# Performance work log

Hardware: AMD Instinct MI355X
Metric: run time of the kernel (lower is better)

The kernel has to match this reference:

```python
import jax, jax.numpy as jnp
import numpy as np

B, T, NF, D, H = 4, 32, 256, 512, 8
DK = D // H


def setup_inputs() -> dict:
    key = jax.random.key(0)
    ks = jax.random.split(key, 10)
    x = jax.random.normal(ks[0], (B, T, NF, D), dtype=jnp.float32)
    adj = jax.random.randint(ks[1], (NF, NF), 0, 2, dtype=jnp.int32)
    adj = adj.at[jnp.arange(NF), jnp.arange(NF)].set(1)  # self-loops avoid all-masked rows
    s = 1.0 / np.sqrt(D)
    Wq = jax.random.normal(ks[2], (D, D), dtype=jnp.float32) * s
    Wk = jax.random.normal(ks[3], (D, D), dtype=jnp.float32) * s
    Wv = jax.random.normal(ks[4], (D, D), dtype=jnp.float32) * s
    Wo = jax.random.normal(ks[5], (D, D), dtype=jnp.float32) * s
    bq = jnp.zeros((D,), jnp.float32)
    bk = jnp.zeros((D,), jnp.float32)
    bv = jnp.zeros((D,), jnp.float32)
    bo = jnp.zeros((D,), jnp.float32)
    return {"x": x, "adj": adj, "Wq": Wq, "bq": bq, "Wk": Wk, "bk": bk,
            "Wv": Wv, "bv": bv, "Wo": Wo, "bo": bo}


def reference(x, adj, Wq, bq, Wk, bk, Wv, bv, Wo, bo):
    b, t, nf, d = x.shape
    q = x @ Wq.T + bq
    k = x @ Wk.T + bk
    v = x @ Wv.T + bv
    # split heads: [B,T,Nf,H,dk]
    qh = q.reshape(b, t, nf, H, DK)
    kh = k.reshape(b, t, nf, H, DK)
    vh = v.reshape(b, t, nf, H, DK)
    scores = jnp.einsum('btihd,btjhd->bthij', qh, kh) / jnp.sqrt(jnp.float32(DK))
    mask = (adj > 0)  # [Nf,Nf], broadcast over b,t,h
    scores = jnp.where(mask[None, None, None], scores, jnp.float32(-jnp.inf))
    attn = jax.nn.softmax(scores, axis=-1)  # dropout is identity in eval
    out = jnp.einsum('bthij,btjhd->btihd', attn, vh).reshape(b, t, nf, d)
    return out @ Wo.T + bo
```

## Files before the change

### kernel.cpp

```cpp
#include <hip/hip_runtime.h>

#define NF 256
#define H_ 8
#define M_ 32768

typedef _Float16 f16;
typedef _Float16 f16x8 __attribute__((ext_vector_type(8)));
typedef float f32x4 __attribute__((ext_vector_type(4)));
typedef unsigned short u16x8 __attribute__((ext_vector_type(8)));
typedef unsigned int u32x2 __attribute__((ext_vector_type(2)));
typedef unsigned int u32x4 __attribute__((ext_vector_type(4)));

#define GLOAD16(src, dst) \
  __builtin_amdgcn_global_load_lds((const __attribute__((address_space(1))) void*)(src), \
                                   (__attribute__((address_space(3))) void*)(dst), 16, 0, 0)

#define LDS_FENCE() do { asm volatile("s_waitcnt lgkmcnt(0)" ::: "memory"); \
                         __builtin_amdgcn_sched_barrier(0); } while (0)
#define SBAR() asm volatile("s_barrier" ::: "memory")


__device__ __forceinline__ void stageHT(const f16* __restrict__ g, int r0, int k0,
                                        f16* ldst, int wave, int lane) {
    const int key = lane >> 3;
    const int colsw = k0 + (((lane & 7) ^ key) << 3);
#pragma unroll
    for (int i = 0; i < 2; ++i) {
        int r = i * 64 + wave * 8 + key;
        GLOAD16(g + (size_t)(r0 + r) * 512 + colsw, ldst + (i * 64 + wave * 8) * 64);
    }
}

__device__ __forceinline__ void gemm256_core(const f16* __restrict__ A, const f16* __restrict__ W,
                                             int m0, int n0, f16* lds,
                                             f32x4 (&acc)[8][4], int wave, int lane) {
    const int wr = wave & 1, wc = wave >> 1;
    const int l15 = lane & 15, l4 = lane >> 4;
    stageHT(W, n0,        0, lds + 16384, wave, lane);
    stageHT(W, n0 + 128,  0, lds + 24576, wave, lane);
    stageHT(A, m0,        0, lds,         wave, lane);
    stageHT(A, m0 + 128,  0, lds + 8192,  wave, lane);
    stageHT(W, n0,       64, lds + 32768 + 16384, wave, lane);
    stageHT(W, n0 + 128, 64, lds + 32768 + 24576, wave, lane);
    asm volatile("s_waitcnt vmcnt(4)" ::: "memory");
    SBAR();
#pragma unroll
    for (int t = 0; t < 8; ++t) {
        f16* bufA = lds + (t & 1) * 32768;
        f16* bufB = bufA + 16384;
        f16* nA   = lds + ((t & 1) ^ 1) * 32768;
        f16x8 bfr[4][2];
#pragma unroll
        for (int j = 0; j < 4; ++j)
#pragma unroll
            for (int kk = 0; kk < 2; ++kk) {
                int rb = wc * 64 + j * 16 + l15;
                bfr[j][kk] = *reinterpret_cast<const f16x8*>(
                    bufB + rb * 64 + ((((kk << 2) + l4) ^ (rb & 7)) << 3));
            }
#pragma unroll
        for (int q = 0; q < 4; ++q) {
            f16x8 afr[2][2];
#pragma unroll
            for (int rf = 0; rf < 2; ++rf)
#pragma unroll
                for (int kk = 0; kk < 2; ++kk) {
                    int ra = wr * 128 + q * 32 + rf * 16 + l15;
                    afr[rf][kk] = *reinterpret_cast<const f16x8*>(
                        bufA + ra * 64 + ((((kk << 2) + l4) ^ (ra & 7)) << 3));
                }
            if (q == 0 && t < 7) stageHT(A, m0,       (t + 1) * 64, nA,          wave, lane);
            if (q == 1 && t < 7) stageHT(A, m0 + 128, (t + 1) * 64, nA + 8192,   wave, lane);
            if (q == 2 && t < 6) stageHT(W, n0,       (t + 2) * 64, bufB,        wave, lane);
            if (q == 3 && t < 6) stageHT(W, n0 + 128, (t + 2) * 64, bufB + 8192, wave, lane);
            SBAR();
            LDS_FENCE();
            __builtin_amdgcn_s_setprio(1);
#pragma unroll
            for (int rf = 0; rf < 2; ++rf)
#pragma unroll
                for (int j = 0; j < 4; ++j)
#pragma unroll
                    for (int kk = 0; kk < 2; ++kk)
                        acc[q * 2 + rf][j] = __builtin_amdgcn_mfma_f32_16x16x32_f16(
                            afr[rf][kk], bfr[j][kk], acc[q * 2 + rf][j], 0, 0, 0);
            __builtin_amdgcn_s_setprio(0);
            if (q < 3) SBAR();
        }
        if (t < 6) { asm volatile("s_waitcnt vmcnt(4)" ::: "memory"); }
        else       { asm volatile("s_waitcnt vmcnt(0)" ::: "memory"); }
        SBAR();
    }
}


#define QSCALE 0.1803368801111204f

__global__ void prep_all(const float* __restrict__ x, f16* __restrict__ xh,
                         const float* __restrict__ Wq, const float* __restrict__ Wk,
                         const float* __restrict__ Wv, const float* __restrict__ Wo,
                         const float* __restrict__ bq, const float* __restrict__ bk,
                         const float* __restrict__ bv, const int* __restrict__ adj,
                         f16* __restrict__ Wh, f16* __restrict__ Woh,
                         float* __restrict__ biasAll, unsigned long long* __restrict__ bmask) {
    if (blockIdx.x < 2048) {
        int idx = blockIdx.x * 256 + threadIdx.x;
        for (; idx < M_ * 512 / 8; idx += 2048 * 256) {
            const float4* s = reinterpret_cast<const float4*>(x + (size_t)idx * 8);
            float4 v0 = s[0], v1 = s[1];
            f16x8 o;
            o[0] = (f16)v0.x; o[1] = (f16)v0.y; o[2] = (f16)v0.z; o[3] = (f16)v0.w;
            o[4] = (f16)v1.x; o[5] = (f16)v1.y; o[6] = (f16)v1.z; o[7] = (f16)v1.w;
            *reinterpret_cast<f16x8*>(xh + (size_t)idx * 8) = o;
        }
        return;
    }
    const int tid = (blockIdx.x - 2048) * 256 + threadIdx.x;
    {
        const float* s; f16* d; float sc = 1.0f;
        int pp = tid >> 15, off = tid & 32767;
        if (pp == 0)      { s = Wq; d = Wh;              sc = QSCALE; }
        else if (pp == 1) { s = Wk; d = Wh + 512 * 512; }
        else if (pp == 2) { s = Wv; d = Wh + 2 * 512 * 512; }
        else              { s = Wo; d = Woh; }
        const float4* sv4 = reinterpret_cast<const float4*>(s + (size_t)off * 8);
        float4 v0 = sv4[0], v1 = sv4[1];
        f16x8 o;
        o[0] = (f16)(v0.x * sc); o[1] = (f16)(v0.y * sc);
        o[2] = (f16)(v0.z * sc); o[3] = (f16)(v0.w * sc);
        o[4] = (f16)(v1.x * sc); o[5] = (f16)(v1.y * sc);
        o[6] = (f16)(v1.z * sc); o[7] = (f16)(v1.w * sc);
        *reinterpret_cast<f16x8*>(d + (size_t)off * 8) = o;
    }
    if (tid < 1536) {
        float v = (tid < 512) ? QSCALE * bq[tid] : (tid < 1024) ? bk[tid - 512] : bv[tid - 1024];
        biasAll[tid] = v;
    }
    if (tid < 65536) {
        unsigned long long bal = __ballot(adj[tid] > 0);
        if ((tid & 63) == 0) bmask[tid >> 6] = bal;
    }
}


__global__ __launch_bounds__(512) void qkv_gemm(const f16* __restrict__ A, const f16* __restrict__ W,
                                                const float* __restrict__ biasAll,
                                                f16* __restrict__ out, f16* __restrict__ vT) {
    __shared__ __align__(16) f16 lds[65536];
    const int tt = threadIdx.x, wave = tt >> 6, lane = tt & 63;
    const int lb = blockIdx.x, xcd = lb & 7, idx = lb >> 3;
    const int m0 = (xcd * 16 + idx / 6) * 256;
    const int n0 = (idx % 6) * 256;
    f32x4 acc[8][4] = {};
    gemm256_core(A, W, m0, n0, lds, acc, wave, lane);

    const int wr = wave & 1, wc = wave >> 1;
    const int l15 = lane & 15, l4 = lane >> 4;
    f16* epi = lds;
    const bool isV = (n0 >= 1024);
    float bb[4];
#pragma unroll
    for (int bc = 0; bc < 4; ++bc) bb[bc] = biasAll[n0 + wc * 64 + bc * 16 + l15];
#pragma unroll
    for (int half = 0; half < 2; ++half) {
        if (wr == half) {
            if (!isV) {
#pragma unroll
                for (int ar = 0; ar < 8; ++ar)
#pragma unroll
                    for (int bc = 0; bc < 4; ++bc)
#pragma unroll
                        for (int r = 0; r < 4; ++r)
                            epi[(ar * 16 + l4 * 4 + r) * 264 + wc * 64 + bc * 16 + l15] =
                                (f16)(acc[ar][bc][r] + bb[bc]);
            } else {
#pragma unroll
                for (int ar = 0; ar < 8; ++ar)
#pragma unroll
                    for (int bc = 0; bc < 4; ++bc)
#pragma unroll
                        for (int r = 0; r < 4; ++r)
                            epi[(wc * 64 + bc * 16 + l15) * 136 + ar * 16 + l4 * 4 + r] =
                                (f16)(acc[ar][bc][r] + bb[bc]);
            }
        }
        LDS_FENCE();
        SBAR();
        if (!isV) {
            const int rr = tt >> 5, slot = tt & 31;
#pragma unroll
            for (int p = 0; p < 8; ++p) {
                int row = p * 16 + rr;
                *reinterpret_cast<f16x8*>(out + (size_t)(m0 + half * 128 + row) * 1024 + n0 + slot * 8) =
                    *reinterpret_cast<const f16x8*>(epi + row * 264 + slot * 8);
            }
        } else {
            f16* vdst = vT + (size_t)(m0 >> 8) * 8 * 64 * 256 + (size_t)(n0 - 1024) * 256;
            const int dk = tt >> 1;
#pragma unroll
            for (int i = 0; i < 8; ++i) {
                int nf0 = (tt & 1) * 64 + i * 8;
                *reinterpret_cast<f16x8*>(vdst + (size_t)dk * 256 + half * 128 + nf0) =
                    *reinterpret_cast<const f16x8*>(epi + dk * 136 + nf0);
            }
        }
        SBAR();
    }
}


template <int NR>
__device__ __forceinline__ void stage_rows512(const f16* __restrict__ g, int ld, int coff,
                                              f16* ldsb, int wave, int lane) {
    const int rr = wave * 8 + (lane >> 3);
    const int p  = lane & 7;
#pragma unroll
    for (int i = 0; i < NR / 64; ++i) {
        int r = i * 64 + rr;
        int col = ((p ^ (r & 7)) << 3);
        GLOAD16(g + (size_t)r * ld + coff + col, ldsb + (i * 64 + wave * 8) * 64);
    }
}

__device__ __forceinline__ void stage_v512(const f16* __restrict__ g, f16* ldsb,
                                           int wave, int lane) {
    const int rr = wave * 8 + (lane >> 3);
    const int p  = lane & 7;
#pragma unroll
    for (int i = 0; i < 4; ++i) {
        int r = i * 64 + rr;
        int key = (r ^ (r >> 3)) & 7;
        GLOAD16(g + (size_t)r * 64 + ((p ^ key) << 3), ldsb + (i * 64 + wave * 8) * 64);
    }
}

__global__ __launch_bounds__(512, 2) void attn_kernel(const f16* __restrict__ qkv,
                                                      const f16* __restrict__ vT,
                                                      const unsigned long long* __restrict__ bmg,
                                                      f16* __restrict__ ao) {
    __shared__ f16 Ks[256 * 64];
    __shared__ f16 Vs[256 * 64];
    __shared__ unsigned long long BMs[1024];
    const int t = threadIdx.x, wave = t >> 6, lane = t & 63;
    const int l15 = lane & 15, l4 = lane >> 4;
    const int bh = blockIdx.x, bt = bh >> 3, h = bh & 7;
    const int btq = bt * 256, hq = h * 64;
    const f16* qb = qkv + (size_t)btq * 1024 + hq;
    const f16* kb = qb + 512;

    stage_rows512<256>(kb, 1024, 0, Ks, wave, lane);
    stage_v512(vT + (size_t)bh * 16384, Vs, wave, lane);
    GLOAD16((const char*)bmg + (size_t)t * 16, (char*)(BMs + wave * 128));
    __syncthreads();

    for (int s = 0; s < 2; ++s) {
        const int qrow_base = wave * 32 + s * 16;

        f16x8 aq[2];
#pragma unroll
        for (int kk = 0; kk < 2; ++kk)
            aq[kk] = *reinterpret_cast<const f16x8*>(
                qb + (size_t)(qrow_base + l15) * 1024 + kk * 32 + l4 * 8);

        f32x4 sc[16];
#pragma unroll
        for (int ct = 0; ct < 16; ++ct) sc[ct] = (f32x4){0.f, 0.f, 0.f, 0.f};
#pragma unroll
        for (int ct = 0; ct < 16; ++ct)
#pragma unroll
            for (int kk = 0; kk < 2; ++kk) {
                int rk = ct * 16 + l15;
                int sk = kk * 4 + l4;
                f16x8 bk_ = *reinterpret_cast<const f16x8*>(Ks + rk * 64 + ((sk ^ (rk & 7)) << 3));
                sc[ct] = __builtin_amdgcn_mfma_f32_16x16x32_f16(bk_, aq[kk], sc[ct], 0, 0, 0);
            }

        float mx = -1e38f;
#pragma unroll
        for (int ct = 0; ct < 16; ++ct)
#pragma unroll
            for (int r = 0; r < 4; ++r) mx = fmaxf(mx, sc[ct][r]);
        mx = fmaxf(mx, __shfl_xor(mx, 16, 64));
        mx = fmaxf(mx, __shfl_xor(mx, 32, 64));

        const int ig = qrow_base + l15;
        const u16x8* mr = reinterpret_cast<const u16x8*>(BMs + ig * 4);
        u16x8 w0 = mr[0], w1 = mr[1];

        f32x4 oacc[4] = {};
        float sum = 0.f;
#pragma unroll
        for (int kkp = 0; kkp < 8; ++kkp) {
            const int ctA = 2 * kkp, ctB = 2 * kkp + 1;
            unsigned mbA = ((kkp < 4) ? (unsigned)w0[ctA] : (unsigned)w1[ctA & 7]) >> (l4 * 4);
            unsigned mbB = ((kkp < 4) ? (unsigned)w0[ctB] : (unsigned)w1[ctB & 7]) >> (l4 * 4);
            float pA0 = __builtin_exp2f(sc[ctA][0] - mx); pA0 = ((mbA >> 0) & 1u) ? pA0 : 0.0f;
            float pA1 = __builtin_exp2f(sc[ctA][1] - mx); pA1 = ((mbA >> 1) & 1u) ? pA1 : 0.0f;
            float pA2 = __builtin_exp2f(sc[ctA][2] - mx); pA2 = ((mbA >> 2) & 1u) ? pA2 : 0.0f;
            float pA3 = __builtin_exp2f(sc[ctA][3] - mx); pA3 = ((mbA >> 3) & 1u) ? pA3 : 0.0f;
            float pB0 = __builtin_exp2f(sc[ctB][0] - mx); pB0 = ((mbB >> 0) & 1u) ? pB0 : 0.0f;
            float pB1 = __builtin_exp2f(sc[ctB][1] - mx); pB1 = ((mbB >> 1) & 1u) ? pB1 : 0.0f;
            float pB2 = __builtin_exp2f(sc[ctB][2] - mx); pB2 = ((mbB >> 2) & 1u) ? pB2 : 0.0f;
            float pB3 = __builtin_exp2f(sc[ctB][3] - mx); pB3 = ((mbB >> 3) & 1u) ? pB3 : 0.0f;
            sum += (pA0 + pA1) + (pA2 + pA3) + (pB0 + pB1) + (pB2 + pB3);
            u32x4 up;
            up[0] = __builtin_bit_cast(unsigned int, __builtin_amdgcn_cvt_pkrtz(pA0, pA1));
            up[1] = __builtin_bit_cast(unsigned int, __builtin_amdgcn_cvt_pkrtz(pA2, pA3));
            up[2] = __builtin_bit_cast(unsigned int, __builtin_amdgcn_cvt_pkrtz(pB0, pB1));
            up[3] = __builtin_bit_cast(unsigned int, __builtin_amdgcn_cvt_pkrtz(pB2, pB3));
            f16x8 pa = __builtin_bit_cast(f16x8, up);
#pragma unroll
            for (int c2 = 0; c2 < 4; ++c2) {
                int d = c2 * 16 + l15;
                int nf0a = kkp * 32 + l4 * 4;
                int nf0b = nf0a + 16;
                int rvA = d * 4 + (nf0a >> 6), rvB = d * 4 + (nf0b >> 6);
                int keyA = (rvA ^ (rvA >> 3)) & 7, keyB = (rvB ^ (rvB >> 3)) & 7;
                u32x2 va = *reinterpret_cast<const u32x2*>(
                    Vs + rvA * 64 + ((((nf0a >> 3) & 7) ^ keyA) << 3) + (nf0a & 7));
                u32x2 vb = *reinterpret_cast<const u32x2*>(
                    Vs + rvB * 64 + ((((nf0b >> 3) & 7) ^ keyB) << 3) + (nf0b & 7));
                u32x4 uv; uv[0] = va[0]; uv[1] = va[1]; uv[2] = vb[0]; uv[3] = vb[1];
                f16x8 bv_ = __builtin_bit_cast(f16x8, uv);
                oacc[c2] = __builtin_amdgcn_mfma_f32_16x16x32_f16(pa, bv_, oacc[c2], 0, 0, 0);
            }
            __builtin_amdgcn_sched_barrier(0);
        }
        sum += __shfl_xor(sum, 16, 64);
        sum += __shfl_xor(sum, 32, 64);
        float rs = 1.0f / sum;
        float rsrow[4];
#pragma unroll
        for (int r = 0; r < 4; ++r) rsrow[r] = __shfl(rs, l4 * 4 + r, 64);

#pragma unroll
        for (int c2 = 0; c2 < 4; ++c2)
#pragma unroll
            for (int r = 0; r < 4; ++r) {
                int nf = qrow_base + l4 * 4 + r;
                int dcol = hq + c2 * 16 + l15;
                ao[((size_t)btq + nf) * 512 + dcol] = (f16)(oacc[c2][r] * rsrow[r]);
            }
    }
}


__global__ __launch_bounds__(512) void o_gemm(const f16* __restrict__ A, const f16* __restrict__ W,
                                              const float* __restrict__ bo, float* __restrict__ out) {
    __shared__ __align__(16) f16 lds[65536];
    const int tt = threadIdx.x, wave = tt >> 6, lane = tt & 63;
    const int lb = blockIdx.x, xcd = lb & 7, idx = lb >> 3;
    const int m0 = (xcd * 16 + idx / 2) * 256;
    const int n0 = (idx % 2) * 256;
    f32x4 acc[8][4] = {};
    gemm256_core(A, W, m0, n0, lds, acc, wave, lane);

    const int wr = wave & 1, wc = wave >> 1;
    const int l15 = lane & 15, l4 = lane >> 4;
    float bb[4];
#pragma unroll
    for (int bc = 0; bc < 4; ++bc) bb[bc] = bo[n0 + wc * 64 + bc * 16 + l15];
#pragma unroll
    for (int ar = 0; ar < 8; ++ar)
#pragma unroll
        for (int bc = 0; bc < 4; ++bc) {
            int ng = n0 + wc * 64 + bc * 16 + l15;
#pragma unroll
            for (int r = 0; r < 4; ++r) {
                int mg = m0 + wr * 128 + ar * 16 + l4 * 4 + r;
                out[(size_t)mg * 512 + ng] = acc[ar][bc][r] + bb[bc];
            }
        }
}


extern "C" void kernel_launch(void* const* d_in, const int* in_sizes, int n_in,
                              void* d_out, int out_size, void* d_ws, size_t ws_size,
                              hipStream_t stream) {
    const float* x   = (const float*)d_in[0];
    const int*   adj = (const int*)d_in[1];
    const float* Wq  = (const float*)d_in[2];
    const float* bq  = (const float*)d_in[3];
    const float* Wk  = (const float*)d_in[4];
    const float* bk  = (const float*)d_in[5];
    const float* Wv  = (const float*)d_in[6];
    const float* bv  = (const float*)d_in[7];
    const float* Wo  = (const float*)d_in[8];
    const float* bo  = (const float*)d_in[9];
    float* out = (float*)d_out;

    char* ws = (char*)d_ws;
    f16*   Wh      = (f16*)ws;
    f16*   Woh     = (f16*)(ws + 1572864);
    float* biasAll = (float*)(ws + 2097152);
    unsigned long long* bmask = (unsigned long long*)(ws + 2103296);
    f16*   xh      = (f16*)(ws + 2111488);
    f16*   qkvb    = (f16*)(ws + 2111488 + (size_t)M_ * 512 * 2);
    f16*   vTb     = (f16*)(ws + 2111488 + (size_t)M_ * 512 * 2 + (size_t)M_ * 1024 * 2);
    f16*   aob     = xh;

    prep_all<<<2560, 256, 0, stream>>>(x, xh, Wq, Wk, Wv, Wo, bq, bk, bv, adj,
                                       Wh, Woh, biasAll, bmask);
    qkv_gemm<<<768, 512, 0, stream>>>(xh, Wh, biasAll, qkvb, vTb);
    attn_kernel<<<128 * H_, 512, 0, stream>>>(qkvb, vTb, bmask, aob);
    o_gemm<<<256, 512, 0, stream>>>(aob, Woh, bo, out);
}
```

Baseline: 171.2 us.

## Halve GEMM K-tile to 32 to cut LDS use and fit two blocks per CU

```diff
diff --git a/kernel.cpp b/kernel.cpp
--- a/kernel.cpp
+++ b/kernel.cpp
@@ -20,15 +20,12 @@
 #define SBAR() asm volatile("s_barrier" ::: "memory")
 
 
-__device__ __forceinline__ void stageHT(const f16* __restrict__ g, int r0, int k0,
-                                        f16* ldst, int wave, int lane) {
-    const int key = lane >> 3;
-    const int colsw = k0 + (((lane & 7) ^ key) << 3);
-#pragma unroll
-    for (int i = 0; i < 2; ++i) {
-        int r = i * 64 + wave * 8 + key;
-        GLOAD16(g + (size_t)(r0 + r) * 512 + colsw, ldst + (i * 64 + wave * 8) * 64);
-    }
+__device__ __forceinline__ void stageHT32(const f16* __restrict__ g, int r0, int k0,
+                                          f16* ldst, int tt) {
+    const int r = tt >> 2;
+    const int p = tt & 3;
+    const int key = (r ^ (r >> 2)) & 3;
+    GLOAD16(g + (size_t)(r0 + r) * 512 + k0 + ((p ^ key) << 3), ldst + r * 32 + p * 8);
 }
 
 __device__ __forceinline__ void gemm256_core(const f16* __restrict__ A, const f16* __restrict__ W,
@@ -36,43 +33,40 @@
                                              f32x4 (&acc)[8][4], int wave, int lane) {
     const int wr = wave & 1, wc = wave >> 1;
     const int l15 = lane & 15, l4 = lane >> 4;
-    stageHT(W, n0,        0, lds + 16384, wave, lane);
-    stageHT(W, n0 + 128,  0, lds + 24576, wave, lane);
-    stageHT(A, m0,        0, lds,         wave, lane);
-    stageHT(A, m0 + 128,  0, lds + 8192,  wave, lane);
-    stageHT(W, n0,       64, lds + 32768 + 16384, wave, lane);
-    stageHT(W, n0 + 128, 64, lds + 32768 + 24576, wave, lane);
-    asm volatile("s_waitcnt vmcnt(4)" ::: "memory");
+    const int tt = wave * 64 + lane;
+    stageHT32(W, n0,        0, lds + 8192,          tt);
+    stageHT32(W, n0 + 128,  0, lds + 8192 + 4096,   tt);
+    stageHT32(A, m0,        0, lds,                 tt);
+    stageHT32(A, m0 + 128,  0, lds + 4096,          tt);
+    stageHT32(W, n0,       32, lds + 16384 + 8192,  tt);
+    stageHT32(W, n0 + 128, 32, lds + 16384 + 12288, tt);
+    asm volatile("s_waitcnt vmcnt(2)" ::: "memory");
     SBAR();
 #pragma unroll
-    for (int t = 0; t < 8; ++t) {
-        f16* bufA = lds + (t & 1) * 32768;
-        f16* bufB = bufA + 16384;
-        f16* nA   = lds + ((t & 1) ^ 1) * 32768;
-        f16x8 bfr[4][2];
-#pragma unroll
-        for (int j = 0; j < 4; ++j)
-#pragma unroll
-            for (int kk = 0; kk < 2; ++kk) {
-                int rb = wc * 64 + j * 16 + l15;
-                bfr[j][kk] = *reinterpret_cast<const f16x8*>(
-                    bufB + rb * 64 + ((((kk << 2) + l4) ^ (rb & 7)) << 3));
-            }
+    for (int t = 0; t < 16; ++t) {
+        f16* bufA = lds + (t & 1) * 16384;
+        f16* bufB = bufA + 8192;
+        f16* nA   = lds + ((t & 1) ^ 1) * 16384;
+        f16x8 bfr[4];
+#pragma unroll
+        for (int j = 0; j < 4; ++j) {
+            int rb = wc * 64 + j * 16 + l15;
+            bfr[j] = *reinterpret_cast<const f16x8*>(
+                bufB + rb * 32 + ((l4 ^ ((rb ^ (rb >> 2)) & 3)) << 3));
+        }
 #pragma unroll
         for (int q = 0; q < 4; ++q) {
-            f16x8 afr[2][2];
-#pragma unroll
-            for (int rf = 0; rf < 2; ++rf)
-#pragma unroll
-                for (int kk = 0; kk < 2; ++kk) {
-                    int ra = wr * 128 + q * 32 + rf * 16 + l15;
-                    afr[rf][kk] = *reinterpret_cast<const f16x8*>(
-                        bufA + ra * 64 + ((((kk << 2) + l4) ^ (ra & 7)) << 3));
-                }
-            if (q == 0 && t < 7) stageHT(A, m0,       (t + 1) * 64, nA,          wave, lane);
-            if (q == 1 && t < 7) stageHT(A, m0 + 128, (t + 1) * 64, nA + 8192,   wave, lane);
-            if (q == 2 && t < 6) stageHT(W, n0,       (t + 2) * 64, bufB,        wave, lane);
-            if (q == 3 && t < 6) stageHT(W, n0 + 128, (t + 2) * 64, bufB + 8192, wave, lane);
+            f16x8 afr[2];
+#pragma unroll
+            for (int rf = 0; rf < 2; ++rf) {
+                int ra = wr * 128 + q * 32 + rf * 16 + l15;
+                afr[rf] = *reinterpret_cast<const f16x8*>(
+                    bufA + ra * 32 + ((l4 ^ ((ra ^ (ra >> 2)) & 3)) << 3));
+            }
+            if (q == 0 && t < 15) stageHT32(A, m0,       (t + 1) * 32, nA,          tt);
+            if (q == 1 && t < 15) stageHT32(A, m0 + 128, (t + 1) * 32, nA + 4096,   tt);
+            if (q == 2 && t < 14) stageHT32(W, n0,       (t + 2) * 32, bufB,        tt);
+            if (q == 3 && t < 14) stageHT32(W, n0 + 128, (t + 2) * 32, bufB + 4096, tt);
             SBAR();
             LDS_FENCE();
             __builtin_amdgcn_s_setprio(1);
@@ -80,15 +74,13 @@
             for (int rf = 0; rf < 2; ++rf)
 #pragma unroll
                 for (int j = 0; j < 4; ++j)
-#pragma unroll
-                    for (int kk = 0; kk < 2; ++kk)
-                        acc[q * 2 + rf][j] = __builtin_amdgcn_mfma_f32_16x16x32_f16(
-                            afr[rf][kk], bfr[j][kk], acc[q * 2 + rf][j], 0, 0, 0);
+                    acc[q * 2 + rf][j] = __builtin_amdgcn_mfma_f32_16x16x32_f16(
+                        afr[rf], bfr[j], acc[q * 2 + rf][j], 0, 0, 0);
             __builtin_amdgcn_s_setprio(0);
             if (q < 3) SBAR();
         }
-        if (t < 6) { asm volatile("s_waitcnt vmcnt(4)" ::: "memory"); }
-        else       { asm volatile("s_waitcnt vmcnt(0)" ::: "memory"); }
+        if (t < 14) { asm volatile("s_waitcnt vmcnt(2)" ::: "memory"); }
+        else        { asm volatile("s_waitcnt vmcnt(0)" ::: "memory"); }
         SBAR();
     }
 }
@@ -146,7 +138,7 @@
 __global__ __launch_bounds__(512) void qkv_gemm(const f16* __restrict__ A, const f16* __restrict__ W,
                                                 const float* __restrict__ biasAll,
                                                 f16* __restrict__ out, f16* __restrict__ vT) {
-    __shared__ __align__(16) f16 lds[65536];
+    __shared__ __align__(16) f16 lds[32768];
     const int tt = threadIdx.x, wave = tt >> 6, lane = tt & 63;
     const int lb = blockIdx.x, xcd = lb & 7, idx = lb >> 3;
     const int m0 = (xcd * 16 + idx / 6) * 256;
@@ -162,46 +154,50 @@
 #pragma unroll
     for (int bc = 0; bc < 4; ++bc) bb[bc] = biasAll[n0 + wc * 64 + bc * 16 + l15];
 #pragma unroll
-    for (int half = 0; half < 2; ++half) {
-        if (wr == half) {
+    for (int c = 0; c < 4; ++c) {
+        if (wr == (c >> 1)) {
             if (!isV) {
 #pragma unroll
-                for (int ar = 0; ar < 8; ++ar)
+                for (int a2 = 0; a2 < 4; ++a2) {
+                    int ar = (c & 1) * 4 + a2;
 #pragma unroll
                     for (int bc = 0; bc < 4; ++bc)
 #pragma unroll
                         for (int r = 0; r < 4; ++r)
-                            epi[(ar * 16 + l4 * 4 + r) * 264 + wc * 64 + bc * 16 + l15] =
+                            epi[(a2 * 16 + l4 * 4 + r) * 264 + wc * 64 + bc * 16 + l15] =
                                 (f16)(acc[ar][bc][r] + bb[bc]);
+                }
             } else {
 #pragma unroll
-                for (int ar = 0; ar < 8; ++ar)
+                for (int a2 = 0; a2 < 4; ++a2) {
+                    int ar = (c & 1) * 4 + a2;
 #pragma unroll
                     for (int bc = 0; bc < 4; ++bc)
 #pragma unroll
                         for (int r = 0; r < 4; ++r)
-                            epi[(wc * 64 + bc * 16 + l15) * 136 + ar * 16 + l4 * 4 + r] =
+                            epi[(wc * 64 + bc * 16 + l15) * 72 + a2 * 16 + l4 * 4 + r] =
                                 (f16)(acc[ar][bc][r] + bb[bc]);
+                }
             }
         }
         LDS_FENCE();
         SBAR();
         if (!isV) {
-            const int rr = tt >> 5, slot = tt & 31;
-#pragma unroll
-            for (int p = 0; p < 8; ++p) {
-                int row = p * 16 + rr;
-                *reinterpret_cast<f16x8*>(out + (size_t)(m0 + half * 128 + row) * 1024 + n0 + slot * 8) =
-                    *reinterpret_cast<const f16x8*>(epi + row * 264 + slot * 8);
+#pragma unroll
+            for (int p = 0; p < 4; ++p) {
+                int row = p * 16 + (tt >> 5);
+                *reinterpret_cast<f16x8*>(
+                    out + (size_t)(m0 + c * 64 + row) * 1024 + n0 + (tt & 31) * 8) =
+                    *reinterpret_cast<const f16x8*>(epi + row * 264 + (tt & 31) * 8);
             }
         } else {
             f16* vdst = vT + (size_t)(m0 >> 8) * 8 * 64 * 256 + (size_t)(n0 - 1024) * 256;
             const int dk = tt >> 1;
 #pragma unroll
-            for (int i = 0; i < 8; ++i) {
-                int nf0 = (tt & 1) * 64 + i * 8;
-                *reinterpret_cast<f16x8*>(vdst + (size_t)dk * 256 + half * 128 + nf0) =
-                    *reinterpret_cast<const f16x8*>(epi + dk * 136 + nf0);
+            for (int i = 0; i < 4; ++i) {
+                int nfl = (tt & 1) * 32 + i * 8;
+                *reinterpret_cast<f16x8*>(vdst + (size_t)dk * 256 + c * 64 + nfl) =
+                    *reinterpret_cast<const f16x8*>(epi + dk * 72 + nfl);
             }
         }
         SBAR();
@@ -347,7 +343,7 @@
 
 __global__ __launch_bounds__(512) void o_gemm(const f16* __restrict__ A, const f16* __restrict__ W,
                                               const float* __restrict__ bo, float* __restrict__ out) {
-    __shared__ __align__(16) f16 lds[65536];
+    __shared__ __align__(16) f16 lds[32768];
     const int tt = threadIdx.x, wave = tt >> 6, lane = tt & 63;
     const int lb = blockIdx.x, xcd = lb & 7, idx = lb >> 3;
     const int m0 = (xcd * 16 + idx / 2) * 256;
```

Result: slower. 176.3 us (+3.0%).
